# Kernel optimization log

Measured on AMD Instinct MI355X. Metric: run time of the kernel, lower is better.

The kernel has to match this reference:

```python
import jax, jax.numpy as jnp
import numpy as np

B, N, K = 4, 4096, 16
C_IN = 128
EPS = 1e-5


def setup_inputs() -> dict:
    key = jax.random.key(0)
    ks = jax.random.split(key, 8)
    c0 = 2 * C_IN + 3  # concat channels: pos_diff(3) + feat2(128) + feat1(128)
    return {
        "pos1": jax.random.normal(ks[0], (B, 3, N), jnp.float32),
        "pos2": jax.random.normal(ks[1], (B, 3, N), jnp.float32),
        "feature1": jax.random.normal(ks[2], (B, C_IN, N), jnp.float32),
        "feature2": jax.random.normal(ks[3], (B, C_IN, N), jnp.float32),
        "W0": jax.random.normal(ks[4], (128, c0), jnp.float32) * 0.05,
        "W1": jax.random.normal(ks[5], (128, 128), jnp.float32) * 0.05,
        "W2": jax.random.normal(ks[6], (128, 128), jnp.float32) * 0.05,
        "g0": jnp.ones((128,), jnp.float32),
        "g1": jnp.ones((128,), jnp.float32),
        "g2": jnp.ones((128,), jnp.float32),
        "b0": jnp.zeros((128,), jnp.float32),
        "b1": jnp.zeros((128,), jnp.float32),
        "b2": jnp.zeros((128,), jnp.float32),
    }


def _knn_idx(pos1, pos2, k):
    # pos1, pos2: (B, 3, N).  For each point in pos1, k nearest points in pos2.
    p1 = pos1.transpose(0, 2, 1)  # (B, N, 3)
    p2 = pos2.transpose(0, 2, 1)  # (B, M, 3)
    d = (jnp.sum(p1 * p1, -1, keepdims=True)
         + jnp.sum(p2 * p2, -1)[:, None, :]
         - 2.0 * jnp.einsum("bnc,bmc->bnm", p1, p2))  # (B, N, M) squared dists
    _, idx = jax.lax.top_k(-d, k)  # (B, N, K)
    return idx


def _group(x, idx):
    # x: (B, C, M), idx: (B, N, K) -> (B, C, N, K)
    xt = x.transpose(0, 2, 1)  # (B, M, C)
    g = jax.vmap(lambda a, i: a[i])(xt, idx)  # (B, N, K, C)
    return g.transpose(0, 3, 1, 2)


def _conv_bn_relu(x, W, g, b):
    # 1x1 conv (no bias) + BatchNorm2d (training: batch stats, biased var) + ReLU
    y = jnp.einsum("oc,bcnk->bonk", W, x)
    mu = jnp.mean(y, axis=(0, 2, 3), keepdims=True)
    var = jnp.var(y, axis=(0, 2, 3), keepdims=True)
    yn = (y - mu) * jax.lax.rsqrt(var + EPS)
    return jax.nn.relu(yn * g[None, :, None, None] + b[None, :, None, None])


def reference(pos1, pos2, feature1, feature2, W0, W1, W2, g0, g1, g2, b0, b1, b2):
    idx = _knn_idx(pos1, pos2, K)                      # (B, N, K)
    pos2_g = _group(pos2, idx)                         # (B, 3, N, K)
    pos_diff = pos2_g - pos1[:, :, :, None]
    feat2_g = _group(feature2, idx)                    # (B, C, N, K)
    feat1_rep = jnp.broadcast_to(feature1[:, :, :, None], (B, C_IN, N, K))
    x = jnp.concatenate([pos_diff, feat2_g, feat1_rep], axis=1)  # (B, 2C+3, N, K)
    x = _conv_bn_relu(x, W0, g0, b0)
    x = _conv_bn_relu(x, W1, g1, b1)
    x = _conv_bn_relu(x, W2, g2, b2)
    feat1_new = jnp.max(x, axis=-1)                    # (B, mlp[-1], N)
    return (pos1, feat1_new)
```

## Files before the change

### kernel.cpp

```cpp
#include <hip/hip_runtime.h>

#define B_ 4
#define N_ 4096
#define K_ 16
#define C_ 128
#define NQ (B_*N_)
#define COLS_TOT (NQ*K_)
#define CNT_F 262144.0f
#define EPS_ 1e-5f

typedef __attribute__((ext_vector_type(8))) short short8;
typedef __attribute__((ext_vector_type(4))) float f4;
typedef __attribute__((ext_vector_type(4))) int i4;
typedef unsigned long long u64;

__device__ __forceinline__ unsigned short f2bf(float f){
  unsigned u = __builtin_bit_cast(unsigned, f);
  u = u + 0x7fffu + ((u >> 16) & 1u);
  return (unsigned short)(u >> 16);
}
__device__ __forceinline__ float bf2f(unsigned short h){
  return __builtin_bit_cast(float, ((unsigned)h) << 16);
}
__device__ __forceinline__ int swzc(int c){ return c ^ ((c >> 3) & 7); }

template<int EXTRA>
__global__ __launch_bounds__(256) void knn_fat(
    const float* __restrict__ pos1, const float* __restrict__ pos2,
    u64* __restrict__ kout, int chunk0,
    const float* __restrict__ W0, const float* __restrict__ W1,
    const float* __restrict__ W2,
    unsigned short* __restrict__ W1b, unsigned short* __restrict__ W2b,
    const float* __restrict__ feat2, const float* __restrict__ feat1,
    float* __restrict__ F2t, float* __restrict__ PREt)
{
  if (EXTRA && blockIdx.x >= 768){
    int i = (blockIdx.x - 768) * 256 + threadIdx.x;
    int sel = i >> 14, r = i & 16383;
    const float* src = sel ? W2 : W1;
    unsigned short* dst = sel ? W2b : W1b;
    dst[r] = f2bf(src[r]);
    return;
  }
  if (EXTRA && blockIdx.x >= 512){
    __shared__ __align__(16) unsigned short X[16*128*8];
    int bid = blockIdx.x - 512;
    int sel = bid >> 7;
    const float* src = sel ? feat1 : feat2;
    float* dst = sel ? PREt : F2t;
    int c0 = (bid & 127) * 128;
    int b = c0 >> 12, mm0 = c0 & 4095;
    int t = threadIdx.x;
    {
      int colt = t & 127, chh = t >> 7;
      #pragma unroll 4
      for (int it = 0; it < 64; ++it){
        int ch = it*2 + chh;
        float v = src[((size_t)b*C_ + ch)*N_ + mm0 + colt];
        X[(ch >> 3)*1024 + swzc(colt)*8 + (ch & 7)] = f2bf(v);
      }
    }
    int lane = t & 63, w = t >> 6;
    int or0 = (w >> 1)*64, c0w = (w & 1)*64;
    int lr = lane & 15, lg = lane >> 4;
    short8 af[4][4];
    #pragma unroll
    for (int ks = 0; ks < 4; ++ks)
      #pragma unroll
      for (int i = 0; i < 4; ++i){
        const float* wr = W0 + (size_t)(or0 + 16*i + lr)*259 + 3 + sel*128
                             + ks*32 + 8*lg;
        f4 lo = *(const f4*)wr, hi = *(const f4*)(wr + 4);
        short8 v;
        #pragma unroll
        for (int e = 0; e < 4; ++e){ v[e] = (short)f2bf(lo[e]); v[e+4] = (short)f2bf(hi[e]); }
        af[ks][i] = v;
      }
    __syncthreads();

    f4 acc[4][4] = {};
    #pragma unroll
    for (int ks = 0; ks < 4; ++ks){
      short8 bfr[4];
      #pragma unroll
      for (int j = 0; j < 4; ++j)
        bfr[j] = *(const short8*)(X + (ks*4 + lg)*1024 + swzc(c0w + 16*j + lr)*8);
      #pragma unroll
      for (int i = 0; i < 4; ++i)
        #pragma unroll
        for (int j = 0; j < 4; ++j)
          acc[i][j] = __builtin_amdgcn_mfma_f32_16x16x32_bf16(af[ks][i], bfr[j], acc[i][j], 0, 0, 0);
    }
    #pragma unroll
    for (int i = 0; i < 4; ++i)
      #pragma unroll
      for (int j = 0; j < 4; ++j){
        int col = c0 + c0w + 16*j + lr;
        *(f4*)(dst + (size_t)col*C_ + or0 + 16*i + 4*lg) = acc[i][j];
      }
    return;
  }
  __shared__ __align__(16) float pts[256*4];
  int bx = blockIdx.x;
  int b = bx >> 7, rest = bx & 127, ngrp = rest >> 3, chunk = chunk0 + (rest & 7);
  int t = threadIdx.x;
  int m0 = chunk * 256;
  const float* p2 = pos2 + (size_t)b*3*N_;
  {
    int m = m0 + t;
    float x = p2[m], y = p2[N_ + m], z = p2[2*N_ + m];
    float sq = __fadd_rn(__fadd_rn(__fmul_rn(x,x), __fmul_rn(y,y)), __fmul_rn(z,z));
    f4 v; v.x = x; v.y = y; v.z = z; v.w = sq;
    *(f4*)(pts + t*4) = v;
  }
  __syncthreads();

  int n = ngrp*256 + t;
  const float* p1 = pos1 + (size_t)b*3*N_;
  float qx = p1[n], qy = p1[N_ + n], qz = p1[2*N_ + n];
  float qs = __fadd_rn(__fadd_rn(__fmul_rn(qx,qx), __fmul_rn(qy,qy)), __fmul_rn(qz,qz));

  u64 list[16];
  #pragma unroll
  for (int j = 0; j < 16; ++j) list[j] = ~0ull;

  #pragma unroll 1
  for (int tile = 0; tile < 16; ++tile){
    u64 tk[16];
    #pragma unroll
    for (int e = 0; e < 16; ++e){
      int it = tile*16 + e;
      f4 c = *(const f4*)(pts + it*4);
      float dot = __builtin_fmaf(qz, c.z,
                    __builtin_fmaf(qy, c.y, __fmul_rn(qx, c.x)));
      float d = __fsub_rn(__fadd_rn(qs, c.w), __fmul_rn(2.0f, dot));
      d = __fadd_rn(d, 0.0f);
      unsigned u = __builtin_bit_cast(unsigned, d);
      u ^= (unsigned)((int)u >> 31) | 0x80000000u;
      tk[e] = ((u64)u << 32) | (unsigned)(m0 + it);
    }
    #pragma unroll
    for (int k = 2; k <= 16; k <<= 1)
      #pragma unroll
      for (int j2 = k >> 1; j2 > 0; j2 >>= 1)
        #pragma unroll
        for (int i = 0; i < 16; ++i){
          int l = i ^ j2;
          if (l > i){
            bool up = ((i & k) == 0);
            u64 a = tk[i], bb = tk[l];
            bool sw = up ? (a > bb) : (a < bb);
            u64 lo = sw ? bb : a, hi = sw ? a : bb;
            tk[i] = lo; tk[l] = hi;
          }
        }
    u64 m16[16];
    #pragma unroll
    for (int i = 0; i < 16; ++i){
      u64 a = list[i], bb = tk[15 - i];
      m16[i] = a < bb ? a : bb;
    }
    #pragma unroll
    for (int j2 = 8; j2 > 0; j2 >>= 1)
      #pragma unroll
      for (int i = 0; i < 16; ++i){
        int l = i ^ j2;
        if (l > i){
          u64 a = m16[i], bb = m16[l];
          bool sw = a > bb;
          m16[i] = sw ? bb : a; m16[l] = sw ? a : bb;
        }
      }
    #pragma unroll
    for (int i = 0; i < 16; ++i) list[i] = m16[i];
  }

  int q = b*N_ + n;
  #pragma unroll
  for (int j = 0; j < 16; ++j)
    kout[(size_t)(chunk*16 + j)*NQ + q] = list[j];
}

__global__ __launch_bounds__(256) void knn_merge(
    const u64* __restrict__ kin, int* __restrict__ idxout)
{
  int q = blockIdx.x*256 + threadIdx.x;
  u64 list[16];
  #pragma unroll
  for (int j = 0; j < 16; ++j) list[j] = ~0ull;
  #pragma unroll 1
  for (int l = 0; l < 16; ++l){
    u64 lv[16];
    #pragma unroll
    for (int j = 0; j < 16; ++j)
      lv[j] = kin[(size_t)(l*16 + j)*NQ + q];
    bool dead = false;
    #pragma unroll
    for (int j = 0; j < 16; ++j){
      bool ins = !dead && (list[15] > lv[j]);
      dead = !ins;
      if (__any(ins)){
        if (ins){
          u64 key = lv[j];
          bool cm = list[14] > key;
          list[15] = cm ? list[14] : key;
          #pragma unroll
          for (int jj = 14; jj >= 1; --jj){
            bool cj = cm;
            cm = list[jj-1] > key;
            list[jj] = cj ? (cm ? list[jj-1] : key) : list[jj];
          }
          list[0] = cm ? key : list[0];
        }
      }
    }
  }
  #pragma unroll
  for (int j = 0; j < 4; ++j){
    i4 v;
    v.x = (int)(list[j*4]   & 0xFFF); v.y = (int)(list[j*4+1] & 0xFFF);
    v.z = (int)(list[j*4+2] & 0xFFF); v.w = (int)(list[j*4+3] & 0xFFF);
    *(i4*)(idxout + (size_t)q*16 + j*4) = v;
  }
}

__global__ __launch_bounds__(256) void k3_stats(
    const float* __restrict__ pos1, const float* __restrict__ pos2,
    const float* __restrict__ W0, const int* __restrict__ idx,
    const float* __restrict__ F2t, const float* __restrict__ PREt,
    float* __restrict__ partials)
{
  __shared__ float w0a[384];
  __shared__ float ldsS[256];
  int t = threadIdx.x;
  for (int i = t; i < 384; i += 256) w0a[i] = W0[(i/3)*259 + (i%3)];
  __syncthreads();
  int cloc = t & 15, chg = t >> 4, ch0 = chg*8;
  float wx[8], wy[8], wz[8];
  #pragma unroll
  for (int e = 0; e < 8; ++e){
    wx[e] = w0a[(ch0+e)*3]; wy[e] = w0a[(ch0+e)*3+1]; wz[e] = w0a[(ch0+e)*3+2];
  }
  float s1[8] = {}, s2[8] = {};
  int base = blockIdx.x * 256;
  for (int it = 0; it < 16; ++it){
    int col = base + it*16 + cloc;
    int nabs = col >> 4;
    int b = nabs >> 12, n = nabs & 4095;
    int m = idx[col];
    float dx = pos2[(size_t)(b*3+0)*N_ + m] - pos1[(size_t)(b*3+0)*N_ + n];
    float dy = pos2[(size_t)(b*3+1)*N_ + m] - pos1[(size_t)(b*3+1)*N_ + n];
    float dz = pos2[(size_t)(b*3+2)*N_ + m] - pos1[(size_t)(b*3+2)*N_ + n];
    const float* f2 = F2t  + ((size_t)b*N_ + m)*C_ + ch0;
    const float* pr = PREt + ((size_t)b*N_ + n)*C_ + ch0;
    #pragma unroll
    for (int e = 0; e < 8; ++e){
      float y = f2[e] + pr[e];
      y = fmaf(wx[e], dx, y); y = fmaf(wy[e], dy, y); y = fmaf(wz[e], dz, y);
      s1[e] += y; s2[e] = fmaf(y, y, s2[e]);
    }
  }
  #pragma unroll
  for (int e = 0; e < 8; ++e){
    float a = s1[e], q = s2[e];
    #pragma unroll
    for (int sft = 1; sft < 16; sft <<= 1){ a += __shfl_xor(a, sft); q += __shfl_xor(q, sft); }
    if (cloc == 0){ ldsS[ch0 + e] = a; ldsS[128 + ch0 + e] = q; }
  }
  __syncthreads();
  partials[(size_t)blockIdx.x*256 + t] = ldsS[t];
}

__global__ __launch_bounds__(256) void redfin(
    const float* __restrict__ partials, float* __restrict__ partial2,
    const float* __restrict__ g, const float* __restrict__ bb,
    float* __restrict__ cA, float* __restrict__ cB,
    int* __restrict__ counter)
{
  __shared__ float sh[256];
  __shared__ int isLast;
  int t = threadIdx.x, blk = blockIdx.x, R = gridDim.x;
  float a = 0.f;
  int r0 = blk*32;
  #pragma unroll 4
  for (int i = 0; i < 32; ++i) a += partials[(size_t)(r0+i)*256 + t];
  partial2[(size_t)blk*256 + t] = a;
  __threadfence();
  if (t == 0){
    int old = atomicAdd(counter, 1);
    isLast = (old == R - 1);
  }
  __syncthreads();
  if (!isLast) return;
  __threadfence();
  float s = 0.f;
  for (int i = 0; i < R; ++i) s += partial2[(size_t)i*256 + t];
  sh[t] = s;
  __syncthreads();
  if (t < 128){
    float mu = sh[t] / CNT_F;
    float var = sh[128 + t] / CNT_F - mu*mu;
    float A = g[t] * rsqrtf(var + EPS_);
    cA[t] = A; cB[t] = bb[t] - mu*A;
  }
  if (t == 0) *counter = 0;
}

__global__ __launch_bounds__(256,2) void layer1_fused(
    const float* __restrict__ pos1, const float* __restrict__ pos2,
    const float* __restrict__ W0, const int* __restrict__ idx,
    const float* __restrict__ F2t, const float* __restrict__ PREt,
    unsigned short* __restrict__ ybuf,
    const unsigned short* __restrict__ Wbf,
    const float* __restrict__ cA, const float* __restrict__ cB,
    float* __restrict__ partials)
{
  __shared__ __align__(16) char lds[40960];
  unsigned short* X = (unsigned short*)lds;
  float* ldsA = (float*)(lds + 32768);
  float* ldsB = ldsA + 128;
  float* w0a  = ldsB + 128;
  float* ldsS = w0a + 384;
  int t = threadIdx.x;
  int c0 = blockIdx.x * 128;
  if (t < 128){ ldsA[t] = cA[t]; ldsB[t] = cB[t]; }
  for (int i = t; i < 384; i += 256) w0a[i] = W0[(i/3)*259 + (i%3)];
  ldsS[t] = 0.f; ldsS[256 + t] = 0.f;
  __syncthreads();

  int lane = t & 63, w = t >> 6;
  int or0 = (w >> 1)*64, c0w = (w & 1)*64;
  int lr = lane & 15, lg = lane >> 4;

  {
    int colL = t >> 1, half = t & 1;
    int col = c0 + colL;
    int nabs = col >> 4;
    int b = nabs >> 12, n = nabs & 4095;
    int m = idx[col];
    float dx = pos2[(size_t)(b*3+0)*N_ + m] - pos1[(size_t)(b*3+0)*N_ + n];
    float dy = pos2[(size_t)(b*3+1)*N_ + m] - pos1[(size_t)(b*3+1)*N_ + n];
    float dz = pos2[(size_t)(b*3+2)*N_ + m] - pos1[(size_t)(b*3+2)*N_ + n];
    const float* f2 = F2t  + ((size_t)b*N_ + m)*C_ + half*64;
    const float* pr = PREt + ((size_t)b*N_ + n)*C_ + half*64;
    int sc = swzc(colL);
    #pragma unroll
    for (int cc = 0; cc < 8; ++cc){
      int ch0 = half*64 + cc*8;
      f4 a0 = *(const f4*)(f2 + cc*8), a1 = *(const f4*)(f2 + cc*8 + 4);
      f4 b0 = *(const f4*)(pr + cc*8), b1 = *(const f4*)(pr + cc*8 + 4);
      short8 xv;
      #pragma unroll
      for (int e = 0; e < 8; ++e){
        int ch = ch0 + e;
        float fv = (e < 4 ? a0[e] : a1[e-4]);
        float pv = (e < 4 ? b0[e] : b1[e-4]);
        float y = fv + pv;
        y = fmaf(w0a[ch*3], dx, y); y = fmaf(w0a[ch*3+1], dy, y); y = fmaf(w0a[ch*3+2], dz, y);
        float v = fmaf(y, ldsA[ch], ldsB[ch]);
        v = v > 0.f ? v : 0.f;
        xv[e] = (short)f2bf(v);
      }
      *(short8*)(X + (ch0 >> 3)*1024 + sc*8) = xv;
    }
  }

  short8 af[4][4];
  #pragma unroll
  for (int ks = 0; ks < 4; ++ks)
    #pragma unroll
    for (int i = 0; i < 4; ++i)
      af[ks][i] = *(const short8*)(Wbf + (or0 + 16*i + lr)*128 + ks*32 + 8*lg);
  __syncthreads();

  f4 acc[4][4] = {};
  #pragma unroll
  for (int ks = 0; ks < 4; ++ks){
    short8 bfr[4];
    #pragma unroll
    for (int j = 0; j < 4; ++j)
      bfr[j] = *(const short8*)(X + (ks*4 + lg)*1024 + swzc(c0w + 16*j + lr)*8);
    #pragma unroll
    for (int i = 0; i < 4; ++i)
      #pragma unroll
      for (int j = 0; j < 4; ++j)
        acc[i][j] = __builtin_amdgcn_mfma_f32_16x16x32_bf16(af[ks][i], bfr[j], acc[i][j], 0, 0, 0);
  }

  #pragma unroll
  for (int i = 0; i < 4; ++i)
    #pragma unroll
    for (int e = 0; e < 4; ++e){
      float a0 = acc[i][0][e], a1 = acc[i][1][e], a2 = acc[i][2][e], a3 = acc[i][3][e];
      float s1 = (a0 + a1) + (a2 + a3);
      float s2 = (a0*a0 + a1*a1) + (a2*a2 + a3*a3);
      #pragma unroll
      for (int sft = 1; sft < 16; sft <<= 1){ s1 += __shfl_xor(s1, sft); s2 += __shfl_xor(s2, sft); }
      if (lr == 0){
        int o = or0 + 16*i + 4*lg + e;
        ldsS[(w & 1)*256 + o] = s1;
        ldsS[(w & 1)*256 + 128 + o] = s2;
      }
    }

  __syncthreads();
  unsigned short* OT = (unsigned short*)lds;
  #pragma unroll
  for (int i = 0; i < 4; ++i)
    #pragma unroll
    for (int j = 0; j < 4; ++j){
      int col = c0w + 16*j + lr;
      int o0 = or0 + 16*i + 4*lg;
      unsigned long long pv =
          (unsigned long long)f2bf(acc[i][j][0])
        | ((unsigned long long)f2bf(acc[i][j][1]) << 16)
        | ((unsigned long long)f2bf(acc[i][j][2]) << 32)
        | ((unsigned long long)f2bf(acc[i][j][3]) << 48);
      *(unsigned long long*)(OT + col*136 + o0) = pv;
    }
  __syncthreads();
  {
    int colL = t >> 1, half = t & 1;
    unsigned short* dst = ybuf + (size_t)(c0 + colL)*128 + half*64;
    #pragma unroll
    for (int cc = 0; cc < 8; ++cc){
      short8 v = *(const short8*)(OT + colL*136 + half*64 + cc*8);
      *(short8*)(dst + cc*8) = v;
    }
  }
  __syncthreads();
  partials[(size_t)blockIdx.x*256 + t] = ldsS[t] + ldsS[256 + t];
}

__global__ __launch_bounds__(256,2) void layer_gemm_last(
    unsigned short* ybuf,
    const unsigned short* __restrict__ Wbf,
    const float* __restrict__ cA, const float* __restrict__ cB,
    float* __restrict__ y2max,
    float* __restrict__ partials)
{
  __shared__ __align__(16) char lds[38912];
  unsigned short* X = (unsigned short*)lds;
  float* ldsA = (float*)(lds + 34816);
  float* ldsB = ldsA + 128;
  float* ldsS = ldsB + 128;
  int t = threadIdx.x;
  int c0 = blockIdx.x * 128;
  if (t < 128){ ldsA[t] = cA[t]; ldsB[t] = cB[t]; }
  ldsS[t] = 0.f; ldsS[256 + t] = 0.f;

  int lane = t & 63, w = t >> 6;
  int or0 = (w >> 1)*64, c0w = (w & 1)*64;
  int lr = lane & 15, lg = lane >> 4;
  short8 af[4][4];
  #pragma unroll
  for (int ks = 0; ks < 4; ++ks)
    #pragma unroll
    for (int i = 0; i < 4; ++i)
      af[ks][i] = *(const short8*)(Wbf + (or0 + 16*i + lr)*128 + ks*32 + 8*lg);
  __syncthreads();

  {
    int colL = t >> 1, half = t & 1;
    const unsigned short* src = ybuf + (size_t)(c0 + colL)*128 + half*64;
    int sc = swzc(colL);
    #pragma unroll
    for (int cc = 0; cc < 8; ++cc){
      int ch0 = half*64 + cc*8;
      short8 yv = *(const short8*)(src + cc*8);
      short8 xv;
      #pragma unroll
      for (int e = 0; e < 8; ++e){
        float f = bf2f((unsigned short)yv[e]);
        float v = fmaf(f, ldsA[ch0 + e], ldsB[ch0 + e]);
        v = v > 0.f ? v : 0.f;
        xv[e] = (short)f2bf(v);
      }
      *(short8*)(X + (ch0 >> 3)*1024 + sc*8) = xv;
    }
  }
  __syncthreads();

  f4 acc[4][4] = {};
  #pragma unroll
  for (int ks = 0; ks < 4; ++ks){
    short8 bfr[4];
    #pragma unroll
    for (int j = 0; j < 4; ++j)
      bfr[j] = *(const short8*)(X + (ks*4 + lg)*1024 + swzc(c0w + 16*j + lr)*8);
    #pragma unroll
    for (int i = 0; i < 4; ++i)
      #pragma unroll
      for (int j = 0; j < 4; ++j)
        acc[i][j] = __builtin_amdgcn_mfma_f32_16x16x32_bf16(af[ks][i], bfr[j], acc[i][j], 0, 0, 0);
  }

  #pragma unroll
  for (int i = 0; i < 4; ++i)
    #pragma unroll
    for (int e = 0; e < 4; ++e){
      float a0 = acc[i][0][e], a1 = acc[i][1][e], a2 = acc[i][2][e], a3 = acc[i][3][e];
      float s1 = (a0 + a1) + (a2 + a3);
      float s2 = (a0*a0 + a1*a1) + (a2*a2 + a3*a3);
      #pragma unroll
      for (int sft = 1; sft < 16; sft <<= 1){ s1 += __shfl_xor(s1, sft); s2 += __shfl_xor(s2, sft); }
      if (lr == 0){
        int o = or0 + 16*i + 4*lg + e;
        ldsS[(w & 1)*256 + o] = s1;
        ldsS[(w & 1)*256 + 128 + o] = s2;
      }
    }

  float keep[4][4] = {};
  #pragma unroll
  for (int j = 0; j < 4; ++j)
    #pragma unroll
    for (int i = 0; i < 4; ++i)
      #pragma unroll
      for (int e = 0; e < 4; ++e){
        float v = acc[i][j][e];
        #pragma unroll
        for (int sft = 1; sft < 16; sft <<= 1) v = fmaxf(v, __shfl_xor(v, sft));
        if (lr == j) keep[i][e] = v;
      }
  if (lr < 4){
    int colg = c0 + c0w + 16*lr;
    int nabs = colg >> 4;
    float* dst = y2max + (size_t)nabs*C_;
    #pragma unroll
    for (int i = 0; i < 4; ++i){
      f4 v; v.x = keep[i][0]; v.y = keep[i][1]; v.z = keep[i][2]; v.w = keep[i][3];
      *(f4*)(dst + or0 + 16*i + 4*lg) = v;
    }
  }
  __syncthreads();
  partials[(size_t)blockIdx.x*256 + t] = ldsS[t] + ldsS[256 + t];
}

__global__ __launch_bounds__(256) void k7_fat(
    const float* __restrict__ y2max, const float* __restrict__ cA,
    const float* __restrict__ cB, float* __restrict__ outF,
    const float* __restrict__ pos1, float* __restrict__ out0)
{
  if (blockIdx.x >= 256){
    int i = ((blockIdx.x - 256)*256 + threadIdx.x)*4;
    *(f4*)(out0 + i) = *(const f4*)(pos1 + i);
    return;
  }
  __shared__ __align__(16) float T[128*65];
  int t = threadIdx.x, bid = blockIdx.x;
  int b = bid >> 6, n0 = (bid & 63)*64;
  {
    int nl = t >> 2, o0 = (t & 3)*32;
    const float* src = y2max + ((size_t)b*N_ + n0 + nl)*C_ + o0;
    #pragma unroll
    for (int jj = 0; jj < 8; ++jj){
      f4 v = *(const f4*)(src + jj*4);
      T[(o0 + jj*4 + 0)*65 + nl] = v.x;
      T[(o0 + jj*4 + 1)*65 + nl] = v.y;
      T[(o0 + jj*4 + 2)*65 + nl] = v.z;
      T[(o0 + jj*4 + 3)*65 + nl] = v.w;
    }
  }
  __syncthreads();
  {
    int o = t >> 1, half = t & 1;
    float A = cA[o], Bb = cB[o];
    float* dst = outF + ((size_t)b*C_ + o)*N_ + n0 + half*32;
    #pragma unroll
    for (int jj = 0; jj < 8; ++jj){
      f4 v;
      float x0 = fmaf(T[o*65 + half*32 + jj*4+0], A, Bb);
      float x1 = fmaf(T[o*65 + half*32 + jj*4+1], A, Bb);
      float x2 = fmaf(T[o*65 + half*32 + jj*4+2], A, Bb);
      float x3 = fmaf(T[o*65 + half*32 + jj*4+3], A, Bb);
      v.x = x0 > 0.f ? x0 : 0.f; v.y = x1 > 0.f ? x1 : 0.f;
      v.z = x2 > 0.f ? x2 : 0.f; v.w = x3 > 0.f ? x3 : 0.f;
      *(f4*)(dst + jj*4) = v;
    }
  }
}

extern "C" void kernel_launch(void* const* d_in, const int* in_sizes, int n_in,
                              void* d_out, int out_size, void* d_ws, size_t ws_size,
                              hipStream_t stream)
{
  (void)in_sizes; (void)n_in; (void)out_size; (void)ws_size;
  const float* pos1  = (const float*)d_in[0];
  const float* pos2  = (const float*)d_in[1];
  const float* feat1 = (const float*)d_in[2];
  const float* feat2 = (const float*)d_in[3];
  const float* W0 = (const float*)d_in[4];
  const float* W1 = (const float*)d_in[5];
  const float* W2 = (const float*)d_in[6];
  const float* g0 = (const float*)d_in[7];
  const float* g1 = (const float*)d_in[8];
  const float* g2 = (const float*)d_in[9];
  const float* b0 = (const float*)d_in[10];
  const float* b1 = (const float*)d_in[11];
  const float* b2 = (const float*)d_in[12];

  char* ws = (char*)d_ws;
  size_t off = 0;
  auto alloc = [&](size_t bytes){ size_t r = off; off += (bytes + 255) & ~(size_t)255; return r; };
  int*   idx     = (int*)  (ws + alloc((size_t)COLS_TOT*4));
  float* F2t     = (float*)(ws + alloc((size_t)NQ*C_*4));
  float* PREt    = (float*)(ws + alloc((size_t)NQ*C_*4));
  unsigned short* ybuf = (unsigned short*)(ws + alloc((size_t)COLS_TOT*C_*2));
  float* y2max   = (float*)(ws + alloc((size_t)NQ*C_*4));
  float* partials= (float*)(ws + alloc((size_t)2048*256*4));
  float* partial2= (float*)(ws + alloc((size_t)64*256*4));
  float* coef    = (float*)(ws + alloc((size_t)6*128*4));
  int*   ctrs    = (int*)  (ws + alloc(256));
  unsigned short* W1b  = (unsigned short*)(ws + alloc(16384*2));
  unsigned short* W2b  = (unsigned short*)(ws + alloc(16384*2));

  u64* knn_k = (u64*)ybuf;

  float* cA0 = coef,       *cB0 = coef + 128;
  float* cA1 = coef + 256, *cB1 = coef + 384;
  float* cA2 = coef + 512, *cB2 = coef + 640;

  hipMemsetAsync(ctrs, 0, 256, stream);
  knn_fat<1><<<896, 256, 0, stream>>>(pos1, pos2, knn_k, 0, W0, W1, W2,
                                       W1b, W2b, feat2, feat1, F2t, PREt);
  knn_fat<0><<<512, 256, 0, stream>>>(pos1, pos2, knn_k, 8, W0, W1, W2,
                                       W1b, W2b, feat2, feat1, F2t, PREt);
  knn_merge<<<64, 256, 0, stream>>>(knn_k, idx);
  k3_stats<<<1024, 256, 0, stream>>>(pos1, pos2, W0, idx, F2t, PREt, partials);
  redfin<<<32, 256, 0, stream>>>(partials, partial2, g0, b0, cA0, cB0, ctrs + 0);
  layer1_fused<<<2048, 256, 0, stream>>>(pos1, pos2, W0, idx, F2t, PREt,
                                          ybuf, W1b, cA0, cB0, partials);
  redfin<<<64, 256, 0, stream>>>(partials, partial2, g1, b1, cA1, cB1, ctrs + 16);
  layer_gemm_last<<<2048, 256, 0, stream>>>(ybuf, W2b, cA1, cB1, y2max, partials);
  redfin<<<64, 256, 0, stream>>>(partials, partial2, g2, b2, cA2, cB2, ctrs + 32);
  k7_fat<<<304, 256, 0, stream>>>(y2max, cA2, cB2,
                                   (float*)d_out + (size_t)B_*3*N_, pos1, (float*)d_out);
}
```

Measured before the change: 370.9 us.

## Merge KNN launches, raise GEMM occupancy, swizzle output LDS staging

Folds the two KNN launches into one 1408-block grid that covers all 16 chunks, saving a launch and the tail gap between them. The two GEMM layer kernels move to launch bounds of 4 blocks per CU with smaller LDS footprints to allow more resident blocks. The layer1 output staging buffer gets an XOR swizzle to reduce LDS bank conflicts. The tighter launch bounds may force register spills.

```diff
diff --git a/kernel.cpp b/kernel.cpp
--- a/kernel.cpp
+++ b/kernel.cpp
@@ -24,27 +24,26 @@
 }
 __device__ __forceinline__ int swzc(int c){ return c ^ ((c >> 3) & 7); }
 
-template<int EXTRA>
-__global__ __launch_bounds__(256) void knn_fat(
+__global__ __launch_bounds__(256) void knn_all(
     const float* __restrict__ pos1, const float* __restrict__ pos2,
-    u64* __restrict__ kout, int chunk0,
+    u64* __restrict__ kout,
     const float* __restrict__ W0, const float* __restrict__ W1,
     const float* __restrict__ W2,
     unsigned short* __restrict__ W1b, unsigned short* __restrict__ W2b,
     const float* __restrict__ feat2, const float* __restrict__ feat1,
     float* __restrict__ F2t, float* __restrict__ PREt)
 {
-  if (EXTRA && blockIdx.x >= 768){
-    int i = (blockIdx.x - 768) * 256 + threadIdx.x;
+  if (blockIdx.x >= 1280){
+    int i = (blockIdx.x - 1280) * 256 + threadIdx.x;
     int sel = i >> 14, r = i & 16383;
     const float* src = sel ? W2 : W1;
     unsigned short* dst = sel ? W2b : W1b;
     dst[r] = f2bf(src[r]);
     return;
   }
-  if (EXTRA && blockIdx.x >= 512){
+  if (blockIdx.x >= 1024){
     __shared__ __align__(16) unsigned short X[16*128*8];
-    int bid = blockIdx.x - 512;
+    int bid = blockIdx.x - 1024;
     int sel = bid >> 7;
     const float* src = sel ? feat1 : feat2;
     float* dst = sel ? PREt : F2t;
@@ -102,7 +101,7 @@
   }
   __shared__ __align__(16) float pts[256*4];
   int bx = blockIdx.x;
-  int b = bx >> 7, rest = bx & 127, ngrp = rest >> 3, chunk = chunk0 + (rest & 7);
+  int b = bx >> 8, rest = bx & 255, ngrp = rest >> 4, chunk = rest & 15;
   int t = threadIdx.x;
   int m0 = chunk * 256;
   const float* p2 = pos2 + (size_t)b*3*N_;
@@ -306,7 +305,7 @@
   if (t == 0) *counter = 0;
 }
 
-__global__ __launch_bounds__(256,2) void layer1_fused(
+__global__ __launch_bounds__(256,4) void layer1_fused(
     const float* __restrict__ pos1, const float* __restrict__ pos2,
     const float* __restrict__ W0, const int* __restrict__ idx,
     const float* __restrict__ F2t, const float* __restrict__ PREt,
@@ -315,12 +314,12 @@
     const float* __restrict__ cA, const float* __restrict__ cB,
     float* __restrict__ partials)
 {
-  __shared__ __align__(16) char lds[40960];
+  __shared__ __align__(16) char lds[37376];
   unsigned short* X = (unsigned short*)lds;
   float* ldsA = (float*)(lds + 32768);
-  float* ldsB = ldsA + 128;
-  float* w0a  = ldsB + 128;
-  float* ldsS = w0a + 384;
+  float* ldsB = (float*)(lds + 33280);
+  float* w0a  = (float*)(lds + 33792);
+  float* ldsS = (float*)(lds + 35328);
   int t = threadIdx.x;
   int c0 = blockIdx.x * 128;
   if (t < 128){ ldsA[t] = cA[t]; ldsB[t] = cB[t]; }
@@ -410,7 +409,7 @@
     #pragma unroll
     for (int j = 0; j < 4; ++j){
       int col = c0w + 16*j + lr;
-      int o0 = or0 + 16*i + 4*lg;
+      int o0 = (or0 + 16*i + 4*lg) ^ ((col & 7) << 4);
       unsigned long long pv =
           (unsigned long long)f2bf(acc[i][j][0])
         | ((unsigned long long)f2bf(acc[i][j][1]) << 16)
@@ -421,10 +420,11 @@
   __syncthreads();
   {
     int colL = t >> 1, half = t & 1;
+    int s = (colL & 7) << 4;
     unsigned short* dst = ybuf + (size_t)(c0 + colL)*128 + half*64;
     #pragma unroll
     for (int cc = 0; cc < 8; ++cc){
-      short8 v = *(const short8*)(OT + colL*136 + half*64 + cc*8);
+      short8 v = *(const short8*)(OT + colL*136 + ((half*64 + cc*8) ^ s));
       *(short8*)(dst + cc*8) = v;
     }
   }
@@ -432,18 +432,18 @@
   partials[(size_t)blockIdx.x*256 + t] = ldsS[t] + ldsS[256 + t];
 }
 
-__global__ __launch_bounds__(256,2) void layer_gemm_last(
+__global__ __launch_bounds__(256,4) void layer_gemm_last(
     unsigned short* ybuf,
     const unsigned short* __restrict__ Wbf,
     const float* __restrict__ cA, const float* __restrict__ cB,
     float* __restrict__ y2max,
     float* __restrict__ partials)
 {
-  __shared__ __align__(16) char lds[38912];
+  __shared__ __align__(16) char lds[35840];
   unsigned short* X = (unsigned short*)lds;
-  float* ldsA = (float*)(lds + 34816);
-  float* ldsB = ldsA + 128;
-  float* ldsS = ldsB + 128;
+  float* ldsA = (float*)(lds + 32768);
+  float* ldsB = (float*)(lds + 33280);
+  float* ldsS = (float*)(lds + 33792);
   int t = threadIdx.x;
   int c0 = blockIdx.x * 128;
   if (t < 128){ ldsA[t] = cA[t]; ldsB[t] = cB[t]; }
@@ -622,10 +622,8 @@
   float* cA2 = coef + 512, *cB2 = coef + 640;
 
   hipMemsetAsync(ctrs, 0, 256, stream);
-  knn_fat<1><<<896, 256, 0, stream>>>(pos1, pos2, knn_k, 0, W0, W1, W2,
-                                       W1b, W2b, feat2, feat1, F2t, PREt);
-  knn_fat<0><<<512, 256, 0, stream>>>(pos1, pos2, knn_k, 8, W0, W1, W2,
-                                       W1b, W2b, feat2, feat1, F2t, PREt);
+  knn_all<<<1408, 256, 0, stream>>>(pos1, pos2, knn_k, W0, W1, W2,
+                                     W1b, W2b, feat2, feat1, F2t, PREt);
   knn_merge<<<64, 256, 0, stream>>>(knn_k, idx);
   k3_stats<<<1024, 256, 0, stream>>>(pos1, pos2, W0, idx, F2t, PREt, partials);
   redfin<<<32, 256, 0, stream>>>(partials, partial2, g0, b0, cA0, cB0, ctrs + 0);
```

After: 390.3 us. +5.2%, slower.
